# Kernel tuning notes

Measured on AMD Instinct MI355X. Metric: run time of the kernel, lower is better.

The kernel has to match this reference:

```python
import jax, jax.numpy as jnp
import numpy as np

B, S, E, H, D = 2, 2048, 1024, 16, 64  # batch, seq(=max_seq_len), embed_dim, heads, atten_dim


def setup_inputs() -> dict:
    key = jax.random.key(0)
    ks = jax.random.split(key, 9)
    s = 0.02
    return {
        "x": jax.random.normal(ks[0], (B, S, E), jnp.float32),
        "Wq": jax.random.normal(ks[1], (H, E, D), jnp.float32) * s,
        "Wk": jax.random.normal(ks[2], (H, E, D), jnp.float32) * s,
        "Wv": jax.random.normal(ks[3], (H, E, D), jnp.float32) * s,
        "bq": jax.random.normal(ks[4], (H, D), jnp.float32) * s,
        "bk": jax.random.normal(ks[5], (H, D), jnp.float32) * s,
        "bv": jax.random.normal(ks[6], (H, D), jnp.float32) * s,
        "Wp": jax.random.normal(ks[7], (H * D, E), jnp.float32) * s,
        "bp": jax.random.normal(ks[8], (E,), jnp.float32) * s,
    }


def reference(x, Wq, Wk, Wv, bq, bk, bv, Wp, bp):
    scale = jnp.sqrt(jnp.float32(D))
    # per-head projections, all heads at once: [B,H,S,D]
    q = jnp.einsum("bse,hed->bhsd", x, Wq) + bq[:, None, :]
    k = jnp.einsum("bse,hed->bhsd", x, Wk) + bk[:, None, :]
    v = jnp.einsum("bse,hed->bhsd", x, Wv) + bv[:, None, :]
    # causal scores [B,H,S,S], additive -inf mask above diagonal (as in the buffer)
    score = jnp.einsum("bhsd,bhtd->bhst", q, k) / scale
    mask = jnp.triu(jnp.full((S, S), -jnp.inf, jnp.float32), k=1)
    score = score + mask
    probs = jax.nn.softmax(score, axis=-1)
    attn = jnp.einsum("bhst,bhtd->bhsd", probs, v)
    # concat heads -> [B,S,H*D], then projection + ReLU
    concat = attn.transpose(0, 2, 1, 3).reshape(B, S, H * D)
    out = jax.nn.relu(concat @ Wp + bp)
    return out
```

## Files before the change

kernel.cpp:

```cpp
#include <hip/hip_runtime.h>

#define S_LEN 2048
#define E_DIM 1024
#define H_NUM 16
#define D_DIM 64

typedef unsigned short u16;
using bf16x8 = __attribute__((ext_vector_type(8))) short;
using f32x4  = __attribute__((ext_vector_type(4))) float;

#define MFMA16(A, B, C) __builtin_amdgcn_mfma_f32_16x16x32_bf16(A, B, C, 0, 0, 0)
#define QSCALE 0.18033688011112042f

__device__ __forceinline__ u16 f2bf(float f) {
    unsigned u = __float_as_uint(f);
    u += 0x7fffu + ((u >> 16) & 1u);
    return (u16)(u >> 16);
}
__device__ __forceinline__ f32x4 fzero4() { f32x4 z; z[0]=0.f; z[1]=0.f; z[2]=0.f; z[3]=0.f; return z; }

__device__ __forceinline__ unsigned cvtpk(float a, float b) {
    unsigned r;
    asm("v_cvt_pk_bf16_f32 %0, %1, %2" : "=v"(r) : "v"(a), "v"(b));
    return r;
}
__device__ __forceinline__ float fexp2(float x) {
#if __has_builtin(__builtin_amdgcn_exp2f)
    return __builtin_amdgcn_exp2f(x);
#else
    float r; asm("v_exp_f32 %0, %1" : "=v"(r) : "v"(x)); return r;
#endif
}
__device__ __forceinline__ float frcp(float x) {
#if __has_builtin(__builtin_amdgcn_rcpf)
    return __builtin_amdgcn_rcpf(x);
#else
    float r; asm("v_rcp_f32 %0, %1" : "=v"(r) : "v"(x)); return r;
#endif
}

__device__ __forceinline__ void gll16(const u16* g, u16* l) {
    __builtin_amdgcn_global_load_lds(
        (const __attribute__((address_space(1))) void*)g,
        (__attribute__((address_space(3))) void*)l, 16, 0, 0);
}

__device__ __forceinline__ void stage64(const u16* __restrict__ g, int gstride,
                                        u16* l, int wave, int lane) {
    #pragma unroll
    for (int i = 0; i < 2; i++) {
        const int r  = wave * 16 + i * 8 + (lane >> 3);
        const int sl = (lane & 7) ^ (r & 7);
        gll16(g + (size_t)r * gstride + sl * 8, l + (wave * 16 + i * 8) * 64);
    }
}
__device__ __forceinline__ bf16x8 ldswz(const u16* t, int rr, int hh, int quad) {
    const int sl = ((hh << 2) + quad) ^ (rr & 7);
    return *(const bf16x8*)(t + rr * 64 + sl * 8);
}

__device__ __forceinline__ void cvt_t_tile(const float* __restrict__ bin, u16* __restrict__ bout,
                                           int R, int C, int r0, int c0) {
    __shared__ float t[64][65];
    const int tid = threadIdx.x;
    const int lr = tid >> 2, lc = (tid & 3) * 16;

    const float* src = bin + (size_t)(r0 + lr) * C + c0 + lc;
    #pragma unroll
    for (int j = 0; j < 4; j++) {
        float4 f = *(const float4*)(src + j * 4);
        t[lr][lc + j * 4 + 0] = f.x; t[lr][lc + j * 4 + 1] = f.y;
        t[lr][lc + j * 4 + 2] = f.z; t[lr][lc + j * 4 + 3] = f.w;
    }
    __syncthreads();

    u16* dst = bout + (size_t)(c0 + lr) * R + r0 + lc;
    u16 vals[16];
    #pragma unroll
    for (int i = 0; i < 16; i++) vals[i] = f2bf(t[lc + i][lr]);
    uint4 pa, pb;
    pa.x = vals[0] | (vals[1] << 16);  pa.y = vals[2] | (vals[3] << 16);
    pa.z = vals[4] | (vals[5] << 16);  pa.w = vals[6] | (vals[7] << 16);
    pb.x = vals[8] | (vals[9] << 16);  pb.y = vals[10] | (vals[11] << 16);
    pb.z = vals[12] | (vals[13] << 16); pb.w = vals[14] | (vals[15] << 16);
    *(uint4*)dst = pa;
    *(uint4*)(dst + 8) = pb;
}

__global__ __launch_bounds__(256) void cvt_all(
    const float* __restrict__ x, u16* __restrict__ xb, int n,
    const float* __restrict__ Wq, const float* __restrict__ Wk, const float* __restrict__ Wv,
    u16* __restrict__ wqt, u16* __restrict__ wkt, u16* __restrict__ wvt,
    const float* __restrict__ Wp, u16* __restrict__ wpt)
{
    const int bid = blockIdx.x;
    if (bid < 4096) {
        int i4 = (bid * 256 + threadIdx.x) * 4;
        if (i4 < n) {
            float4 f = *(const float4*)(x + i4);
            unsigned lo = (unsigned)f2bf(f.x) | ((unsigned)f2bf(f.y) << 16);
            unsigned hi = (unsigned)f2bf(f.z) | ((unsigned)f2bf(f.w) << 16);
            uint2 p; p.x = lo; p.y = hi;
            *(uint2*)(xb + i4) = p;
        }
    } else if (bid < 4096 + 768) {
        const int t  = bid - 4096;
        const int z  = t >> 4;
        const int ry = t & 15;
        const int which = z >> 4, bh = z & 15;
        const float* in = (which == 0) ? Wq : (which == 1) ? Wk : Wv;
        u16* outp = (which == 0) ? wqt : (which == 1) ? wkt : wvt;
        cvt_t_tile(in + (size_t)bh * E_DIM * D_DIM, outp + (size_t)bh * E_DIM * D_DIM,
                   E_DIM, D_DIM, ry * 64, 0);
    } else {
        const int t = bid - (4096 + 768);
        cvt_t_tile(Wp, wpt, H_NUM * D_DIM, E_DIM, (t >> 4) * 64, (t & 15) * 64);
    }
}

__global__ __launch_bounds__(128, 2) void qkv_gemm(
    const u16* __restrict__ xb, const u16* __restrict__ wcat,
    const float* __restrict__ bq, const float* __restrict__ bk, const float* __restrict__ bv,
    u16* __restrict__ oq, u16* __restrict__ okk, u16* __restrict__ ov)
{
    const int m0 = blockIdx.x * 128;
    const int n0 = blockIdx.y * 128;

    __shared__ u16 As[2][64 * 64];
    __shared__ u16 Bs[2][64 * 64];

    const int tid  = threadIdx.x;
    const int wave = tid >> 6, lane = tid & 63, quad = lane >> 4, l16 = lane & 15;

    f32x4 acc[8][4];
    #pragma unroll
    for (int j = 0; j < 8; j++)
        #pragma unroll
        for (int mi = 0; mi < 4; mi++) acc[j][mi] = fzero4();

#define STAGE(K0, BUF)                                                               \
    _Pragma("unroll")                                                                \
    for (int i = 0; i < 2; i++) {                                                    \
        const int r  = wave * 32 + i * 8 + (lane >> 3);           \
        const int s  = (lane & 7) ^ (r & 7);                      \
        const int mr = r + ((s >> 2) << 6);                      \
        const int kc = (s & 3) * 8;                              \
        gll16(xb   + (size_t)(m0 + mr) * E_DIM + (K0) + kc,                          \
              &As[BUF][(wave * 32 + i * 8) * 64]);                                   \
        gll16(wcat + (size_t)(n0 + mr) * E_DIM + (K0) + kc,                          \
              &Bs[BUF][(wave * 32 + i * 8) * 64]);                                   \
        const int r2  = wave * 32 + 16 + i * 8 + (lane >> 3);                        \
        const int s2  = (lane & 7) ^ (r2 & 7);                                       \
        const int mr2 = r2 + ((s2 >> 2) << 6);                                       \
        const int kc2 = (s2 & 3) * 8;                                                \
        gll16(xb   + (size_t)(m0 + mr2) * E_DIM + (K0) + kc2,                        \
              &As[BUF][(wave * 32 + 16 + i * 8) * 64]);                              \
        gll16(wcat + (size_t)(n0 + mr2) * E_DIM + (K0) + kc2,                        \
              &Bs[BUF][(wave * 32 + 16 + i * 8) * 64]);                              \
    }

    STAGE(0, 0);

    for (int kt = 0; kt < 32; kt++) {
        __syncthreads();
        if (kt < 31) {
            const int kn = (kt + 1) * 32;
            if ((kt & 1) == 0) { STAGE(kn, 1); } else { STAGE(kn, 0); }
        }
        const u16* Ac = As[kt & 1];
        const u16* Bc = Bs[kt & 1];

        bf16x8 af[4];
        #pragma unroll
        for (int mi = 0; mi < 4; mi++) {
            const int row = mi * 16 + l16;
            af[mi] = *(const bf16x8*)(&Ac[row * 64 + ((((wave << 2) + quad)) ^ (row & 7)) * 8]);
        }
        __builtin_amdgcn_s_setprio(1);
        #pragma unroll
        for (int j = 0; j < 8; j++) {
            const int row = (j & 3) * 16 + l16;
            bf16x8 bfv = *(const bf16x8*)(&Bc[row * 64 +
                              ((((j >> 2) << 2) + quad) ^ (row & 7)) * 8]);
            #pragma unroll
            for (int mi = 0; mi < 4; mi++)
                acc[j][mi] = MFMA16(af[mi], bfv, acc[j][mi]);
        }
        __builtin_amdgcn_s_setprio(0);
    }
#undef STAGE

    const int t = n0 >> 10;
    if (t < 2) {
        const float scl = (t == 0) ? QSCALE : 1.0f;
        const float* bias = (t == 0) ? bq : bk;
        u16* dst = (t == 0) ? oq : okk;
        #pragma unroll
        for (int j = 0; j < 8; j++) {
            const int n = n0 + j * 16 + l16;
            const int h = (n >> 6) & 15, d = n & 63;
            float bia = bias[h * D_DIM + d];
            #pragma unroll
            for (int mi = 0; mi < 4; mi++) {
                #pragma unroll
                for (int r = 0; r < 4; r++) {
                    int m = m0 + wave * 64 + mi * 16 + quad * 4 + r;
                    int b = m >> 11, s = m & 2047;
                    dst[((size_t)(b * H_NUM + h) * S_LEN + s) * D_DIM + d] =
                        f2bf((acc[j][mi][r] + bia) * scl);
                }
            }
        }
    } else {
        const int b  = m0 >> 11, s0 = m0 & 2047;
        const int h0 = (n0 >> 6) & 15;
        u16* Tb0 = &As[0][0];
        u16* Tb1 = &Bs[0][0];
        #pragma unroll
        for (int pass = 0; pass < 2; ++pass) {
            __syncthreads();
            if (wave == pass) {
                #pragma unroll
                for (int j = 0; j < 8; j++) {
                    const int n = n0 + j * 16 + l16;
                    const int d = n & 63, hh = (n >> 6) & 15;
                    const float bia = bv[hh * D_DIM + d];
                    u16* Tb = (j < 4) ? Tb0 : Tb1;
                    const int nl = (j & 3) * 16 + l16;
                    #pragma unroll
                    for (int mi = 0; mi < 4; mi++) {
                        uint2 pk;
                        pk.x = cvtpk(acc[j][mi][0] + bia, acc[j][mi][1] + bia);
                        pk.y = cvtpk(acc[j][mi][2] + bia, acc[j][mi][3] + bia);
                        *(uint2*)(&Tb[nl * 72 + mi * 16 + quad * 4]) = pk;
                    }
                }
            }
            __syncthreads();
            #pragma unroll
            for (int g = 0; g < 8; ++g) {
                const int rowi = g * 16 + (tid >> 3);
                const int ml = (tid & 7) * 8;
                const u16* srcp = (rowi < 64 ? Tb0 : Tb1) + (rowi & 63) * 72 + ml;
                const int hh = h0 + (rowi >> 6), d = rowi & 63;
                u16* dstp = ov + ((size_t)(b * H_NUM + hh) * D_DIM + d) * S_LEN
                               + s0 + pass * 64 + ml;
                *(uint4*)dstp = *(const uint4*)srcp;
            }
        }
    }
}

__global__ __launch_bounds__(256, 2) void attn_fwd(
    const u16* __restrict__ q, const u16* __restrict__ k, const u16* __restrict__ vt,
    u16* __restrict__ concat)
{
    const int bid  = blockIdx.x;
    const int halfg = bid >> 8;
    const int pi   = (bid & 255) >> 5;
    const int p    = halfg ? (15 - pi) : pi;
    const int g    = bid & 31;
    const int h    = g & 15;
    const int bb   = g >> 4;
    const int qa = p, qb = 31 - p;

    const size_t headoff = (size_t)(bb * H_NUM + h) * S_LEN * D_DIM;
    const u16* qh  = q  + headoff;
    const u16* kh  = k  + headoff;
    const u16* vth = vt + headoff;

    __shared__ u16 QaL[64 * 64];
    __shared__ u16 QbL[64 * 64];
    __shared__ u16 Ks[2][64 * 64];
    __shared__ u16 Vts[2][64 * 64];
    __shared__ u16 Psa[4][16 * 72];
    __shared__ u16 Psb[4][16 * 72];

    const int tid  = threadIdx.x;
    const int wave = tid >> 6, lane = tid & 63, quad = lane >> 4, l16 = lane & 15;

    stage64(qh + (size_t)qa * 64 * D_DIM, D_DIM, QaL,    wave, lane);
    stage64(qh + (size_t)qb * 64 * D_DIM, D_DIM, QbL,    wave, lane);
    stage64(kh,                           D_DIM, Ks[0],  wave, lane);
    stage64(vth,                          S_LEN, Vts[0], wave, lane);
    __syncthreads();

    bf16x8 bqa0 = ldswz(QaL, wave * 16 + l16, 0, quad);
    bf16x8 bqa1 = ldswz(QaL, wave * 16 + l16, 1, quad);
    bf16x8 bqb0 = ldswz(QbL, wave * 16 + l16, 0, quad);
    bf16x8 bqb1 = ldswz(QbL, wave * 16 + l16, 1, quad);

    f32x4 oa[4], ob[4];
    #pragma unroll
    for (int nt = 0; nt < 4; nt++) { oa[nt] = fzero4(); ob[nt] = fzero4(); }
    float la = 0.f, lb = 0.f;

    const int qga = qa * 64 + wave * 16 + l16;
    const int qgb = qb * 64 + wave * 16 + l16;

    u16* pwa = &Psa[wave][0];
    u16* pwb = &Psb[wave][0];

    for (int kt = 0; kt <= qb; kt++) {
        __syncthreads();
        if (kt < qb) {
            stage64(kh + (size_t)(kt + 1) * 64 * D_DIM, D_DIM, Ks[(kt + 1) & 1],  wave, lane);
            stage64(vth + (kt + 1) * 64,                S_LEN, Vts[(kt + 1) & 1], wave, lane);
        }
        const u16* Kc = Ks[kt & 1];
        const u16* Vc = Vts[kt & 1];
        const bool both = (kt <= qa);

        f32x4 stb[4], sta[4];
        __builtin_amdgcn_s_setprio(1);
        #pragma unroll
        for (int nt = 0; nt < 4; nt++) {
            const int rr = nt * 16 + l16;
            bf16x8 ak0 = ldswz(Kc, rr, 0, quad);
            bf16x8 ak1 = ldswz(Kc, rr, 1, quad);
            stb[nt] = MFMA16(ak0, bqb0, fzero4());
            stb[nt] = MFMA16(ak1, bqb1, stb[nt]);
            if (both) {
                sta[nt] = MFMA16(ak0, bqa0, fzero4());
                sta[nt] = MFMA16(ak1, bqa1, sta[nt]);
            }
        }
        __builtin_amdgcn_s_setprio(0);

        bf16x8 bv0[4], bv1[4];
        #pragma unroll
        for (int nt = 0; nt < 4; nt++) {
            bv0[nt] = ldswz(Vc, nt * 16 + l16, 0, quad);
            bv1[nt] = ldswz(Vc, nt * 16 + l16, 1, quad);
        }

        #pragma unroll
        for (int nt = 0; nt < 4; nt++) {
            float pe[4];
            if (kt == qb) {
                #pragma unroll
                for (int r = 0; r < 4; r++) {
                    int kkg = kt * 64 + nt * 16 + quad * 4 + r;
                    pe[r] = (kkg > qgb) ? 0.f : fexp2(stb[nt][r]);
                }
            } else {
                #pragma unroll
                for (int r = 0; r < 4; r++) pe[r] = fexp2(stb[nt][r]);
            }
            lb += (pe[0] + pe[1]) + (pe[2] + pe[3]);
            uint2 pk;
            pk.x = cvtpk(pe[0], pe[1]);
            pk.y = cvtpk(pe[2], pe[3]);
            *(uint2*)(&pwb[l16 * 72 + nt * 16 + quad * 4]) = pk;
        }
        if (both) {
            #pragma unroll
            for (int nt = 0; nt < 4; nt++) {
                float pe[4];
                if (kt == qa) {
                    #pragma unroll
                    for (int r = 0; r < 4; r++) {
                        int kkg = kt * 64 + nt * 16 + quad * 4 + r;
                        pe[r] = (kkg > qga) ? 0.f : fexp2(sta[nt][r]);
                    }
                } else {
                    #pragma unroll
                    for (int r = 0; r < 4; r++) pe[r] = fexp2(sta[nt][r]);
                }
                la += (pe[0] + pe[1]) + (pe[2] + pe[3]);
                uint2 pk;
                pk.x = cvtpk(pe[0], pe[1]);
                pk.y = cvtpk(pe[2], pe[3]);
                *(uint2*)(&pwa[l16 * 72 + nt * 16 + quad * 4]) = pk;
            }
        }

        {
            bf16x8 ap0 = *(const bf16x8*)(&pwb[l16 * 72 + quad * 8]);
            bf16x8 ap1 = *(const bf16x8*)(&pwb[l16 * 72 + 32 + quad * 8]);
            __builtin_amdgcn_s_setprio(1);
            #pragma unroll
            for (int nt = 0; nt < 4; nt++) {
                ob[nt] = MFMA16(ap0, bv0[nt], ob[nt]);
                ob[nt] = MFMA16(ap1, bv1[nt], ob[nt]);
            }
            __builtin_amdgcn_s_setprio(0);
        }
        if (both) {
            bf16x8 ap0 = *(const bf16x8*)(&pwa[l16 * 72 + quad * 8]);
            bf16x8 ap1 = *(const bf16x8*)(&pwa[l16 * 72 + 32 + quad * 8]);
            __builtin_amdgcn_s_setprio(1);
            #pragma unroll
            for (int nt = 0; nt < 4; nt++) {
                oa[nt] = MFMA16(ap0, bv0[nt], oa[nt]);
                oa[nt] = MFMA16(ap1, bv1[nt], oa[nt]);
            }
            __builtin_amdgcn_s_setprio(0);
        }
    }

    lb += __shfl_xor(lb, 16); lb += __shfl_xor(lb, 32);
    la += __shfl_xor(la, 16); la += __shfl_xor(la, 32);

    #pragma unroll
    for (int r = 0; r < 4; r++) {
        const int srcl = quad * 4 + r;
        float lbi = frcp(__shfl(lb, srcl));
        float lai = frcp(__shfl(la, srcl));
        int sqa = qa * 64 + wave * 16 + quad * 4 + r;
        int sqb = qb * 64 + wave * 16 + quad * 4 + r;
        #pragma unroll
        for (int nt = 0; nt < 4; nt++) {
            concat[((size_t)(bb * S_LEN + sqa)) * E_DIM + h * D_DIM + nt * 16 + l16] =
                f2bf(oa[nt][r] * lai);
            concat[((size_t)(bb * S_LEN + sqb)) * E_DIM + h * D_DIM + nt * 16 + l16] =
                f2bf(ob[nt][r] * lbi);
        }
    }
}

__global__ __launch_bounds__(256, 2) void out_proj(
    const u16* __restrict__ concat, const u16* __restrict__ wpt,
    const float* __restrict__ bp, float* __restrict__ out)
{
    const int bid = blockIdx.x;
    const int mt  = (bid & 7) * 8 + ((bid >> 3) & 7);
    const int nt0 = bid >> 6;
    const int m0 = mt * 64;
    const int n0 = nt0 * 128;

    __shared__ u16 As[2][64 * 64];
    __shared__ u16 Bs[2][128 * 64];

    const int tid  = threadIdx.x;
    const int wave = tid >> 6, lane = tid & 63, quad = lane >> 4, l16 = lane & 15;
    const int mh = wave >> 1, nh = wave & 1;

    f32x4 acc[4][2];
    #pragma unroll
    for (int j = 0; j < 4; j++)
        #pragma unroll
        for (int mi = 0; mi < 2; mi++) acc[j][mi] = fzero4();

    stage64(concat + (size_t)m0 * E_DIM, E_DIM, As[0], wave, lane);
    stage64(wpt + (size_t)n0 * E_DIM,        E_DIM, Bs[0],           wave, lane);
    stage64(wpt + (size_t)(n0 + 64) * E_DIM, E_DIM, Bs[0] + 64 * 64, wave, lane);

    for (int kt = 0; kt < 16; kt++) {
        __syncthreads();
        if (kt < 15) {
            const int k0 = (kt + 1) * 64;
            u16* an = As[(kt + 1) & 1];
            u16* bn = Bs[(kt + 1) & 1];
            stage64(concat + (size_t)m0 * E_DIM + k0, E_DIM, an, wave, lane);
            stage64(wpt + (size_t)n0 * E_DIM + k0,        E_DIM, bn,           wave, lane);
            stage64(wpt + (size_t)(n0 + 64) * E_DIM + k0, E_DIM, bn + 64 * 64, wave, lane);
        }
        const u16* Ac = As[kt & 1];
        const u16* Bc = Bs[kt & 1];

        #pragma unroll
        for (int kq = 0; kq < 2; kq++) {
            bf16x8 af[2];
            #pragma unroll
            for (int mi = 0; mi < 2; mi++)
                af[mi] = ldswz(Ac, mh * 32 + mi * 16 + l16, kq, quad);
            __builtin_amdgcn_s_setprio(1);
            #pragma unroll
            for (int j = 0; j < 4; j++) {
                bf16x8 bfv = ldswz(Bc, nh * 64 + j * 16 + l16, kq, quad);
                #pragma unroll
                for (int mi = 0; mi < 2; mi++)
                    acc[j][mi] = MFMA16(af[mi], bfv, acc[j][mi]);
            }
            __builtin_amdgcn_s_setprio(0);
        }
    }

    #pragma unroll
    for (int j = 0; j < 4; j++) {
        int n = n0 + nh * 64 + j * 16 + l16;
        float bia = bp[n];
        #pragma unroll
        for (int mi = 0; mi < 2; mi++) {
            #pragma unroll
            for (int r = 0; r < 4; r++) {
                int m = m0 + mh * 32 + mi * 16 + quad * 4 + r;
                out[(size_t)m * E_DIM + n] = fmaxf(acc[j][mi][r] + bia, 0.f);
            }
        }
    }
}

extern "C" void kernel_launch(void* const* d_in, const int* in_sizes, int n_in,
                              void* d_out, int out_size, void* d_ws, size_t ws_size,
                              hipStream_t stream)
{
    (void)in_sizes; (void)n_in; (void)out_size; (void)ws_size;
    const float* x  = (const float*)d_in[0];
    const float* Wq = (const float*)d_in[1];
    const float* Wk = (const float*)d_in[2];
    const float* Wv = (const float*)d_in[3];
    const float* bq = (const float*)d_in[4];
    const float* bk = (const float*)d_in[5];
    const float* bv = (const float*)d_in[6];
    const float* Wp = (const float*)d_in[7];
    const float* bp = (const float*)d_in[8];
    float* out = (float*)d_out;

    const size_t QKV_ELEMS = (size_t)2 * H_NUM * S_LEN * D_DIM;
    const size_t W_ELEMS   = (size_t)H_NUM * E_DIM * D_DIM;

    u16* q   = (u16*)d_ws;
    u16* k   = q   + QKV_ELEMS;
    u16* v   = k   + QKV_ELEMS;
    u16* cc  = v   + QKV_ELEMS;
    u16* xb  = cc  + QKV_ELEMS;
    u16* wqt = xb  + QKV_ELEMS;
    u16* wkt = wqt + W_ELEMS;
    u16* wvt = wkt + W_ELEMS;
    u16* wpt = wvt + W_ELEMS;

    cvt_all<<<dim3(4096 + 768 + 256), 256, 0, stream>>>(
        x, xb, (int)QKV_ELEMS, Wq, Wk, Wv, wqt, wkt, wvt, Wp, wpt);

    qkv_gemm<<<dim3(32, 24), 128, 0, stream>>>(xb, wqt, bq, bk, bv, q, k, v);
    attn_fwd<<<dim3(512), 256, 0, stream>>>(q, k, v, cc);
    out_proj<<<dim3(512), 256, 0, stream>>>(cc, wpt, bp, out);
}
```

Before: 175.3 us.

## Use 32x32 MFMA attention with register-only P via permlane32 swap

Rewrites the causal attention kernel so that each pair of waves owns one 64-row query tile (qb or qa), with 32 query rows per wave, and uses 32x32x16 bf16 MFMAs instead of 16x16x32. The softmax probabilities are packed into MFMA A-operands in registers with v_permlane32_swap rather than going through an LDS round trip. Q fragments are staged through the K/V buffers, which frees the Q and P shared arrays. Waves working on the shorter qa tile skip iterations once past their diagonal, so work within a block becomes unbalanced between wave pairs. This trades lower LDS traffic and fewer instructions for a longer critical path in the qb waves.

New measurement: 178.5 us. About the same (+1.8%).

```diff
diff --git a/kernel.cpp b/kernel.cpp
--- a/kernel.cpp
+++ b/kernel.cpp
@@ -8,8 +8,10 @@
 typedef unsigned short u16;
 using bf16x8 = __attribute__((ext_vector_type(8))) short;
 using f32x4  = __attribute__((ext_vector_type(4))) float;
+using f32x16 = __attribute__((ext_vector_type(16))) float;
 
 #define MFMA16(A, B, C) __builtin_amdgcn_mfma_f32_16x16x32_bf16(A, B, C, 0, 0, 0)
+#define MFMA32(A, B, C) __builtin_amdgcn_mfma_f32_32x32x16_bf16(A, B, C, 0, 0, 0)
 #define QSCALE 0.18033688011112042f
 
 __device__ __forceinline__ u16 f2bf(float f) {
@@ -18,6 +20,12 @@
     return (u16)(u >> 16);
 }
 __device__ __forceinline__ f32x4 fzero4() { f32x4 z; z[0]=0.f; z[1]=0.f; z[2]=0.f; z[3]=0.f; return z; }
+__device__ __forceinline__ f32x16 fzero16() {
+    f32x16 z;
+    #pragma unroll
+    for (int i = 0; i < 16; i++) z[i] = 0.f;
+    return z;
+}
 
 __device__ __forceinline__ unsigned cvtpk(float a, float b) {
     unsigned r;
@@ -57,6 +65,9 @@
 __device__ __forceinline__ bf16x8 ldswz(const u16* t, int rr, int hh, int quad) {
     const int sl = ((hh << 2) + quad) ^ (rr & 7);
     return *(const bf16x8*)(t + rr * 64 + sl * 8);
+}
+__device__ __forceinline__ bf16x8 ldfr(const u16* t, int rr, int sl) {
+    return *(const bf16x8*)(t + rr * 64 + ((sl ^ (rr & 7)) * 8));
 }
 
 __device__ __forceinline__ void cvt_t_tile(const float* __restrict__ bin, u16* __restrict__ bout,
@@ -260,162 +271,126 @@
     const int pi   = (bid & 255) >> 5;
     const int p    = halfg ? (15 - pi) : pi;
     const int g    = bid & 31;
-    const int h    = g & 15;
+    const int hd   = g & 15;
     const int bb   = g >> 4;
     const int qa = p, qb = 31 - p;
 
-    const size_t headoff = (size_t)(bb * H_NUM + h) * S_LEN * D_DIM;
-    const u16* qh  = q  + headoff;
-    const u16* kh  = k  + headoff;
-    const u16* vth = vt + headoff;
-
-    __shared__ u16 QaL[64 * 64];
-    __shared__ u16 QbL[64 * 64];
+    const size_t headoff = (size_t)(bb * H_NUM + hd) * S_LEN * D_DIM;
+    const u16* qptr = q  + headoff;
+    const u16* kptr = k  + headoff;
+    const u16* vptr = vt + headoff;
+
     __shared__ u16 Ks[2][64 * 64];
     __shared__ u16 Vts[2][64 * 64];
-    __shared__ u16 Psa[4][16 * 72];
-    __shared__ u16 Psb[4][16 * 72];
+    __shared__ float Ls[4][32];
 
     const int tid  = threadIdx.x;
-    const int wave = tid >> 6, lane = tid & 63, quad = lane >> 4, l16 = lane & 15;
-
-    stage64(qh + (size_t)qa * 64 * D_DIM, D_DIM, QaL,    wave, lane);
-    stage64(qh + (size_t)qb * 64 * D_DIM, D_DIM, QbL,    wave, lane);
-    stage64(kh,                           D_DIM, Ks[0],  wave, lane);
-    stage64(vth,                          S_LEN, Vts[0], wave, lane);
+    const int wave = tid >> 6, lane = tid & 63;
+    const int l32 = lane & 31, hh = lane >> 5;
+
+    const int mytile = (wave >> 1) ? qa : qb;
+    const int qhalf  = wave & 1;
+
+    stage64(qptr + (size_t)qb * 64 * D_DIM, D_DIM, Ks[0],  wave, lane);
+    stage64(qptr + (size_t)qa * 64 * D_DIM, D_DIM, Vts[0], wave, lane);
     __syncthreads();
 
-    bf16x8 bqa0 = ldswz(QaL, wave * 16 + l16, 0, quad);
-    bf16x8 bqa1 = ldswz(QaL, wave * 16 + l16, 1, quad);
-    bf16x8 bqb0 = ldswz(QbL, wave * 16 + l16, 0, quad);
-    bf16x8 bqb1 = ldswz(QbL, wave * 16 + l16, 1, quad);
-
-    f32x4 oa[4], ob[4];
-    #pragma unroll
-    for (int nt = 0; nt < 4; nt++) { oa[nt] = fzero4(); ob[nt] = fzero4(); }
-    float la = 0.f, lb = 0.f;
-
-    const int qga = qa * 64 + wave * 16 + l16;
-    const int qgb = qb * 64 + wave * 16 + l16;
-
-    u16* pwa = &Psa[wave][0];
-    u16* pwb = &Psb[wave][0];
+    bf16x8 qf[4];
+    {
+        const u16* Qsrc = (wave >> 1) ? &Vts[0][0] : &Ks[0][0];
+        const int row = qhalf * 32 + l32;
+        #pragma unroll
+        for (int c = 0; c < 4; c++) qf[c] = ldfr(Qsrc, row, c * 2 + hh);
+    }
+    __syncthreads();
+
+    stage64(kptr, D_DIM, Ks[0],  wave, lane);
+    stage64(vptr, S_LEN, Vts[0], wave, lane);
+
+    f32x16 o0 = fzero16(), o1 = fzero16();
+    float ls = 0.f;
+    const int qg   = mytile * 64 + qhalf * 32 + l32;
+    const int kk4h = 4 * hh;
 
     for (int kt = 0; kt <= qb; kt++) {
         __syncthreads();
         if (kt < qb) {
-            stage64(kh + (size_t)(kt + 1) * 64 * D_DIM, D_DIM, Ks[(kt + 1) & 1],  wave, lane);
-            stage64(vth + (kt + 1) * 64,                S_LEN, Vts[(kt + 1) & 1], wave, lane);
-        }
-        const u16* Kc = Ks[kt & 1];
-        const u16* Vc = Vts[kt & 1];
-        const bool both = (kt <= qa);
-
-        f32x4 stb[4], sta[4];
+            stage64(kptr + (size_t)(kt + 1) * 64 * D_DIM, D_DIM, Ks[(kt + 1) & 1],  wave, lane);
+            stage64(vptr + (kt + 1) * 64,                 S_LEN, Vts[(kt + 1) & 1], wave, lane);
+        }
+        if (kt > mytile) continue;
+
+        const u16* Kc = &Ks[kt & 1][0];
+        const u16* Vc = &Vts[kt & 1][0];
+
+        f32x16 s0 = fzero16(), s1 = fzero16();
         __builtin_amdgcn_s_setprio(1);
         #pragma unroll
-        for (int nt = 0; nt < 4; nt++) {
-            const int rr = nt * 16 + l16;
-            bf16x8 ak0 = ldswz(Kc, rr, 0, quad);
-            bf16x8 ak1 = ldswz(Kc, rr, 1, quad);
-            stb[nt] = MFMA16(ak0, bqb0, fzero4());
-            stb[nt] = MFMA16(ak1, bqb1, stb[nt]);
-            if (both) {
-                sta[nt] = MFMA16(ak0, bqa0, fzero4());
-                sta[nt] = MFMA16(ak1, bqa1, sta[nt]);
+        for (int c = 0; c < 4; c++) {
+            bf16x8 ak0 = ldfr(Kc, l32,      c * 2 + hh);
+            bf16x8 ak1 = ldfr(Kc, 32 + l32, c * 2 + hh);
+            s0 = MFMA32(ak0, qf[c], s0);
+            s1 = MFMA32(ak1, qf[c], s1);
+        }
+        __builtin_amdgcn_s_setprio(0);
+
+        float pe0[16], pe1[16];
+        if (kt == mytile) {
+            #pragma unroll
+            for (int r = 0; r < 16; r++) {
+                const int kkg = kt * 64 + (r & 3) + 8 * (r >> 2) + kk4h;
+                pe0[r] = (kkg      > qg) ? 0.f : fexp2(s0[r]);
+                pe1[r] = (kkg + 32 > qg) ? 0.f : fexp2(s1[r]);
             }
+        } else {
+            #pragma unroll
+            for (int r = 0; r < 16; r++) { pe0[r] = fexp2(s0[r]); pe1[r] = fexp2(s1[r]); }
+        }
+        #pragma unroll
+        for (int r = 0; r < 16; r++) ls += pe0[r] + pe1[r];
+
+        bf16x8 pa[4];
+#define BUILD_PA(PE, D0, D1)                                                      \
+        {                                                                         \
+            unsigned X0 = cvtpk(PE[0], PE[1]),   X1 = cvtpk(PE[2], PE[3]);        \
+            unsigned Y0 = cvtpk(PE[4], PE[5]),   Y1 = cvtpk(PE[6], PE[7]);        \
+            asm("v_permlane32_swap_b32 %0, %1" : "+v"(X0), "+v"(Y0));             \
+            asm("v_permlane32_swap_b32 %0, %1" : "+v"(X1), "+v"(Y1));             \
+            int4 f0; f0.x = (int)X0; f0.y = (int)X1; f0.z = (int)Y0; f0.w = (int)Y1; \
+            D0 = *(bf16x8*)&f0;                                                   \
+            unsigned Z0 = cvtpk(PE[8], PE[9]),   Z1 = cvtpk(PE[10], PE[11]);      \
+            unsigned W0 = cvtpk(PE[12], PE[13]), W1 = cvtpk(PE[14], PE[15]);      \
+            asm("v_permlane32_swap_b32 %0, %1" : "+v"(Z0), "+v"(W0));             \
+            asm("v_permlane32_swap_b32 %0, %1" : "+v"(Z1), "+v"(W1));             \
+            int4 f1; f1.x = (int)Z0; f1.y = (int)Z1; f1.z = (int)W0; f1.w = (int)W1; \
+            D1 = *(bf16x8*)&f1;                                                   \
+        }
+        BUILD_PA(pe0, pa[0], pa[1]);
+        BUILD_PA(pe1, pa[2], pa[3]);
+#undef BUILD_PA
+
+        __builtin_amdgcn_s_setprio(1);
+        #pragma unroll
+        for (int j = 0; j < 4; j++) {
+            bf16x8 bv0 = ldfr(Vc, l32,      j * 2 + hh);
+            bf16x8 bv1 = ldfr(Vc, 32 + l32, j * 2 + hh);
+            o0 = MFMA32(pa[j], bv0, o0);
+            o1 = MFMA32(pa[j], bv1, o1);
         }
         __builtin_amdgcn_s_setprio(0);
-
-        bf16x8 bv0[4], bv1[4];
-        #pragma unroll
-        for (int nt = 0; nt < 4; nt++) {
-            bv0[nt] = ldswz(Vc, nt * 16 + l16, 0, quad);
-            bv1[nt] = ldswz(Vc, nt * 16 + l16, 1, quad);
-        }
-
-        #pragma unroll
-        for (int nt = 0; nt < 4; nt++) {
-            float pe[4];
-            if (kt == qb) {
-                #pragma unroll
-                for (int r = 0; r < 4; r++) {
-                    int kkg = kt * 64 + nt * 16 + quad * 4 + r;
-                    pe[r] = (kkg > qgb) ? 0.f : fexp2(stb[nt][r]);
-                }
-            } else {
-                #pragma unroll
-                for (int r = 0; r < 4; r++) pe[r] = fexp2(stb[nt][r]);
-            }
-            lb += (pe[0] + pe[1]) + (pe[2] + pe[3]);
-            uint2 pk;
-            pk.x = cvtpk(pe[0], pe[1]);
-            pk.y = cvtpk(pe[2], pe[3]);
-            *(uint2*)(&pwb[l16 * 72 + nt * 16 + quad * 4]) = pk;
-        }
-        if (both) {
-            #pragma unroll
-            for (int nt = 0; nt < 4; nt++) {
-                float pe[4];
-                if (kt == qa) {
-                    #pragma unroll
-                    for (int r = 0; r < 4; r++) {
-                        int kkg = kt * 64 + nt * 16 + quad * 4 + r;
-                        pe[r] = (kkg > qga) ? 0.f : fexp2(sta[nt][r]);
-                    }
-                } else {
-                    #pragma unroll
-                    for (int r = 0; r < 4; r++) pe[r] = fexp2(sta[nt][r]);
-                }
-                la += (pe[0] + pe[1]) + (pe[2] + pe[3]);
-                uint2 pk;
-                pk.x = cvtpk(pe[0], pe[1]);
-                pk.y = cvtpk(pe[2], pe[3]);
-                *(uint2*)(&pwa[l16 * 72 + nt * 16 + quad * 4]) = pk;
-            }
-        }
-
-        {
-            bf16x8 ap0 = *(const bf16x8*)(&pwb[l16 * 72 + quad * 8]);
-            bf16x8 ap1 = *(const bf16x8*)(&pwb[l16 * 72 + 32 + quad * 8]);
-            __builtin_amdgcn_s_setprio(1);
-            #pragma unroll
-            for (int nt = 0; nt < 4; nt++) {
-                ob[nt] = MFMA16(ap0, bv0[nt], ob[nt]);
-                ob[nt] = MFMA16(ap1, bv1[nt], ob[nt]);
-            }
-            __builtin_amdgcn_s_setprio(0);
-        }
-        if (both) {
-            bf16x8 ap0 = *(const bf16x8*)(&pwa[l16 * 72 + quad * 8]);
-            bf16x8 ap1 = *(const bf16x8*)(&pwa[l16 * 72 + 32 + quad * 8]);
-            __builtin_amdgcn_s_setprio(1);
-            #pragma unroll
-            for (int nt = 0; nt < 4; nt++) {
-                oa[nt] = MFMA16(ap0, bv0[nt], oa[nt]);
-                oa[nt] = MFMA16(ap1, bv1[nt], oa[nt]);
-            }
-            __builtin_amdgcn_s_setprio(0);
-        }
-    }
-
-    lb += __shfl_xor(lb, 16); lb += __shfl_xor(lb, 32);
-    la += __shfl_xor(la, 16); la += __shfl_xor(la, 32);
-
-    #pragma unroll
-    for (int r = 0; r < 4; r++) {
-        const int srcl = quad * 4 + r;
-        float lbi = frcp(__shfl(lb, srcl));
-        float lai = frcp(__shfl(la, srcl));
-        int sqa = qa * 64 + wave * 16 + quad * 4 + r;
-        int sqb = qb * 64 + wave * 16 + quad * 4 + r;
-        #pragma unroll
-        for (int nt = 0; nt < 4; nt++) {
-            concat[((size_t)(bb * S_LEN + sqa)) * E_DIM + h * D_DIM + nt * 16 + l16] =
-                f2bf(oa[nt][r] * lai);
-            concat[((size_t)(bb * S_LEN + sqb)) * E_DIM + h * D_DIM + nt * 16 + l16] =
-                f2bf(ob[nt][r] * lbi);
-        }
+    }
+
+    ls += __shfl_xor(ls, 32);
+    if (hh == 0) Ls[wave][l32] = ls;
+
+    #pragma unroll
+    for (int r = 0; r < 16; r++) {
+        const int qlr = (r & 3) + 8 * (r >> 2) + kk4h;
+        const float li = frcp(Ls[wave][qlr]);
+        const int qrow = mytile * 64 + qhalf * 32 + qlr;
+        u16* dst = concat + ((size_t)(bb * S_LEN + qrow)) * E_DIM + hd * D_DIM;
+        dst[l32]      = f2bf(o0[r] * li);
+        dst[32 + l32] = f2bf(o1[r] * li);
     }
 }
 
```
